# Kernel tuning notes

Measured on AMD Instinct MI355X. Metric: run time of the kernel, lower is better.

## Reference

```python
import jax, jax.numpy as jnp
import numpy as np

N_NODES = 500_000
N_EDGES = 16_000_000
D_COEF = 1  # init arg d
EPS = 1e-12  # F.normalize eps


def setup_inputs() -> dict:
    key = jax.random.key(0)
    k1, k2, k3 = jax.random.split(key, 3)
    theta = jax.random.normal(k1, (N_NODES, 1), dtype=jnp.float32)
    src = jax.random.randint(k2, (N_EDGES,), 0, N_NODES, dtype=jnp.int64)
    dst = jax.random.randint(k3, (N_EDGES,), 0, N_NODES, dtype=jnp.int64)
    v0 = jnp.ones((), dtype=jnp.float32)
    w0 = jnp.ones((), dtype=jnp.float32)
    return {"theta": theta, "src": src, "dst": dst, "v0": v0, "w0": w0}


def reference(theta, src, dst, v0, w0):
    # node velocity: v0 * [cos(theta), sin(theta)]  -> [N, 2]
    v = v0 * jnp.concatenate((jnp.cos(theta), jnp.sin(theta)), axis=-1)

    # edge message: dtheta = (theta_src - theta_dst) * d ; m = [cos, sin] -> [E, 2]
    dtheta = (theta[src, 0] - theta[dst, 0]) * D_COEF  # [E]
    m = jnp.stack((jnp.cos(dtheta), jnp.sin(dtheta)), axis=-1)  # [E, 2]

    # mailbox mean over incoming edges per destination node (segment mean)
    msum = jax.ops.segment_sum(m, dst, num_segments=N_NODES)  # [N, 2]
    cnt = jax.ops.segment_sum(jnp.ones((dst.shape[0],), m.dtype), dst,
                              num_segments=N_NODES)  # [N]
    mean_cs = msum / jnp.maximum(cnt, 1.0)[:, None]  # [N, 2]

    # torque: w0 * normalize(mean_cs, dim=-1)[..., 1:2]
    norm = jnp.linalg.norm(mean_cs, axis=-1, keepdims=True)
    unit = mean_cs / jnp.maximum(norm, EPS)
    torque = w0 * unit[:, 1:2]  # [N, 1]
    return v, torque
```

## Files before the change

kernel.cpp:

```cpp
#include <hip/hip_runtime.h>
#include <hip/hip_bf16.h>
#include <math.h>


#define NBITS_Q   21
#define Q_MASK    ((1u << NBITS_Q) - 1)
#define Q_SCALE   131072.0f
#define Q_INV     (1.0f / 131072.0f)
#define BIN_SHIFT 11
#define BIN_W     2048
#define NB        245
#define CAP       67584
#define K_BATCH   8192
#define EPT       8
#define SCALE_F   524288.0f
#define INV_SCALE (1.0f / 524288.0f)

__global__ void init_cursors(unsigned* __restrict__ cur) {
    int b = blockIdx.x * blockDim.x + threadIdx.x;
    if (b < 256) cur[b] = (b < NB) ? (unsigned)b * CAP : 0u;
}

__global__ __launch_bounds__(1024, 8) void bin_edges_sort(
        const float* __restrict__ theta,
        const int4* __restrict__ src4, const int4* __restrict__ dst4,
        unsigned* __restrict__ bins, unsigned* __restrict__ cursor, int E)
{
    __shared__ unsigned      sorted[K_BATCH];
    __shared__ unsigned char sbin[K_BATCH];
    __shared__ unsigned      hist[256];
    __shared__ unsigned      base[256];
    __shared__ unsigned      gbase[256];
    __shared__ unsigned      lcnt[256];

    const int tid   = threadIdx.x;
    const int bb    = blockIdx.x;
    const int e0    = bb * K_BATCH;
    const int nval  = min(K_BATCH, E - e0);
    const int E4    = E >> 2;
    const int base4 = e0 >> 2;

    if (tid < 256) { hist[tid] = 0u; lcnt[tid] = 0u; }
    __syncthreads();

    int4 sQ[EPT / 4], dQ[EPT / 4];
#pragma unroll
    for (int j = 0; j < EPT / 4; ++j) {
        const int idx4 = base4 + j * 1024 + tid;
        if (idx4 < E4) {
            sQ[j] = src4[idx4];
            dQ[j] = dst4[idx4];
        } else {
            sQ[j] = make_int4(0, 0, 0, 0);
            dQ[j] = make_int4(0, 0, 0, 0);
        }
    }
    float tq[EPT];
#pragma unroll
    for (int j = 0; j < EPT / 4; ++j) {
        tq[j * 4 + 0] = theta[sQ[j].x];
        tq[j * 4 + 1] = theta[sQ[j].y];
        tq[j * 4 + 2] = theta[sQ[j].z];
        tq[j * 4 + 3] = theta[sQ[j].w];
    }

    unsigned ent[EPT];
    unsigned bn[EPT];
#pragma unroll
    for (int j = 0; j < EPT / 4; ++j) {
        const int idx4 = base4 + j * 1024 + tid;
        const int q0   = j * 4;
        if (idx4 < E4) {
            const int dd[4] = {dQ[j].x, dQ[j].y, dQ[j].z, dQ[j].w};
#pragma unroll
            for (int k = 0; k < 4; ++k) {
                const unsigned b = (unsigned)dd[k] >> BIN_SHIFT;
                float qf = (tq[q0 + k] + 8.0f) * Q_SCALE + 0.5f;
                qf = fminf(fmaxf(qf, 0.0f), 2097151.0f);
                ent[q0 + k] = ((unsigned)(dd[k] & (BIN_W - 1)) << NBITS_Q)
                              | (unsigned)qf;
                bn[q0 + k]  = b;
                atomicAdd(&hist[b], 1u);
            }
        } else {
#pragma unroll
            for (int k = 0; k < 4; ++k) bn[q0 + k] = 0xFFu;
        }
    }
    __syncthreads();

    if (tid < 64) {
        unsigned h[4];
#pragma unroll
        for (int k = 0; k < 4; ++k) h[k] = hist[tid * 4 + k];
        const unsigned tot = h[0] + h[1] + h[2] + h[3];
        unsigned s = tot;
#pragma unroll
        for (int off = 1; off < 64; off <<= 1) {
            const unsigned y = __shfl_up(s, off);
            if (tid >= off) s += y;
        }
        unsigned run = s - tot;
#pragma unroll
        for (int k = 0; k < 4; ++k) {
            base[tid * 4 + k] = run;
            run += h[k];
        }
#pragma unroll
        for (int k = 0; k < 4; ++k)
            if (h[k]) gbase[tid * 4 + k] = atomicAdd(&cursor[tid * 4 + k], h[k]);
    }
    __syncthreads();

#pragma unroll
    for (int q = 0; q < EPT; ++q) {
        if (bn[q] != 0xFFu) {
            const unsigned b   = bn[q];
            const unsigned pos = base[b] + atomicAdd(&lcnt[b], 1u);
            sorted[pos] = ent[q];
            sbin[pos]   = (unsigned char)b;
        }
    }
    __syncthreads();

    for (int l = tid; l < nval; l += 1024) {
        const unsigned b    = sbin[l];
        const unsigned gpos = gbase[b] + ((unsigned)l - base[b]);
        if (gpos < (b + 1u) * CAP)
            bins[gpos] = sorted[l];
    }
}

__global__ __launch_bounds__(1024) void reduce_bins(
        const float* __restrict__ theta, const unsigned* __restrict__ bins,
        const unsigned* __restrict__ cursor, const float* __restrict__ v0p,
        const float* __restrict__ w0p, float* __restrict__ out, int N)
{
    __shared__ float th[BIN_W];
    __shared__ unsigned long long acc[BIN_W];
    const int b     = blockIdx.x;
    const int tid   = threadIdx.x;
    const int node0 = b * BIN_W;
    const int W     = min(BIN_W, N - node0);

    for (int j = tid; j < BIN_W; j += 1024) {
        th[j]  = (j < W) ? theta[node0 + j] : 0.f;
        acc[j] = 0ull;
    }
    __syncthreads();

    const unsigned  base  = (unsigned)b * CAP;
    const int       count = (int)(cursor[b] - base);
    const unsigned* bp    = bins + base;

    const int CH = 1024 * 8;
    int i0 = 0;
    for (; i0 + CH <= count; i0 += CH) {
        const uint4 ea = *(const uint4*)(bp + i0 + tid * 4);
        const uint4 eb = *(const uint4*)(bp + i0 + 4096 + tid * 4);
        const unsigned ee[8] = {ea.x, ea.y, ea.z, ea.w, eb.x, eb.y, eb.z, eb.w};
#pragma unroll
        for (int k = 0; k < 8; ++k) {
            const unsigned e = ee[k];
            const unsigned l = e >> NBITS_Q;
            const float ts = (float)(e & Q_MASK) * Q_INV - 8.0f;
            float sn, cs;
            __sincosf(ts - th[l], &sn, &cs);
            const unsigned cq = (unsigned)((cs + 1.0f) * SCALE_F + 0.5f);
            const unsigned sq = (unsigned)((sn + 1.0f) * SCALE_F + 0.5f);
            atomicAdd(&acc[l], (1ull << 56) | ((unsigned long long)cq << 28)
                               | (unsigned long long)sq);
        }
    }
    for (int i = i0 + tid; i < count; i += 1024) {
        const unsigned e = bp[i];
        const unsigned l = e >> NBITS_Q;
        const float ts = (float)(e & Q_MASK) * Q_INV - 8.0f;
        float sn, cs;
        __sincosf(ts - th[l], &sn, &cs);
        const unsigned cq = (unsigned)((cs + 1.0f) * SCALE_F + 0.5f);
        const unsigned sq = (unsigned)((sn + 1.0f) * SCALE_F + 0.5f);
        atomicAdd(&acc[l], (1ull << 56) | ((unsigned long long)cq << 28)
                           | (unsigned long long)sq);
    }
    __syncthreads();

    const float v0 = *v0p, w0 = *w0p;
    for (int j = tid; j < W; j += 1024) {
        const float t = th[j];
        float sn, cs;
        __sincosf(t, &sn, &cs);
        ((float2*)out)[node0 + j] = make_float2(v0 * cs, v0 * sn);
        const unsigned long long P = acc[j];
        const float c  = (float)(unsigned)(P >> 56);
        const float xs = (float)(unsigned)((P >> 28) & 0xFFFFFFFull) * INV_SCALE - c;
        const float ys = (float)(unsigned)(P & 0xFFFFFFFull) * INV_SCALE - c;
        const float nrm = sqrtf(xs * xs + ys * ys);
        out[2 * N + node0 + j] = w0 * (ys / fmaxf(nrm, 1e-12f));
    }
}


__global__ void zero_ws_kernel(float4* __restrict__ ws, int n4) {
    int i = blockIdx.x * blockDim.x + threadIdx.x;
    if (i < n4) ws[i] = make_float4(0.f, 0.f, 0.f, 0.f);
}

__global__ void edge_kernel_fb(const float* __restrict__ theta,
                               const int4* __restrict__ src4,
                               const int4* __restrict__ dst4,
                               float2* __restrict__ acc, int E8) {
    int i = blockIdx.x * blockDim.x + threadIdx.x;
    if (i >= E8) return;
    const int4 s0 = src4[2 * i], s1 = src4[2 * i + 1];
    const int4 d0 = dst4[2 * i], d1 = dst4[2 * i + 1];
    const int ss[8] = {s0.x, s0.y, s0.z, s0.w, s1.x, s1.y, s1.z, s1.w};
    const int dd[8] = {d0.x, d0.y, d0.z, d0.w, d1.x, d1.y, d1.z, d1.w};
    float ts[8], td[8];
#pragma unroll
    for (int k = 0; k < 8; ++k) ts[k] = theta[ss[k]];
#pragma unroll
    for (int k = 0; k < 8; ++k) td[k] = theta[dd[k]];
#pragma unroll
    for (int k = 0; k < 8; ++k) {
        float sn, cs;
        __sincosf(ts[k] - td[k], &sn, &cs);
        atomicAdd(&acc[dd[k]].x, cs);
        atomicAdd(&acc[dd[k]].y, sn);
    }
}

__global__ void node_kernel_fb(const float* __restrict__ theta,
                               const float2* __restrict__ acc,
                               const float* __restrict__ v0p,
                               const float* __restrict__ w0p,
                               float* __restrict__ out, int N) {
    int i = blockIdx.x * blockDim.x + threadIdx.x;
    if (i >= N) return;
    const float v0 = *v0p, w0 = *w0p;
    float sn, cs;
    __sincosf(theta[i], &sn, &cs);
    ((float2*)out)[i] = make_float2(v0 * cs, v0 * sn);
    const float2 a = acc[i];
    const float nrm = sqrtf(a.x * a.x + a.y * a.y);
    out[2 * N + i] = w0 * (a.y / fmaxf(nrm, 1e-12f));
}

extern "C" void kernel_launch(void* const* d_in, const int* in_sizes, int n_in,
                              void* d_out, int out_size, void* d_ws, size_t ws_size,
                              hipStream_t stream) {
    const float* theta = (const float*)d_in[0];
    const int*   src   = (const int*)d_in[1];
    const int*   dst   = (const int*)d_in[2];
    const float* v0p   = (const float*)d_in[3];
    const float* w0p   = (const float*)d_in[4];
    float*       out   = (float*)d_out;

    const int N = in_sizes[0];
    const int E = in_sizes[1];

    const size_t need = 1024 + (size_t)NB * CAP * sizeof(unsigned);

    if (ws_size >= need && N <= NB * BIN_W) {
        unsigned* cursor = (unsigned*)d_ws;
        unsigned* bins   = cursor + 256;

        init_cursors<<<1, 256, 0, stream>>>(cursor);

        const int nblk = (E + K_BATCH - 1) / K_BATCH;
        bin_edges_sort<<<nblk, 1024, 0, stream>>>(theta, (const int4*)src,
                                                  (const int4*)dst,
                                                  bins, cursor, E);

        const int nbins = (N + BIN_W - 1) / BIN_W;
        reduce_bins<<<nbins, 1024, 0, stream>>>(theta, bins, cursor,
                                                v0p, w0p, out, N);
    } else {
        float2* acc = (float2*)d_ws;
        {
            const int n4 = (2 * N) / 4;
            zero_ws_kernel<<<(n4 + 255) / 256, 256, 0, stream>>>((float4*)d_ws, n4);
        }
        {
            const int E8 = E / 8;
            edge_kernel_fb<<<(E8 + 255) / 256, 256, 0, stream>>>(
                theta, (const int4*)src, (const int4*)dst, acc, E8);
        }
        node_kernel_fb<<<(N + 255) / 256, 256, 0, stream>>>(theta, acc, v0p, w0p,
                                                            out, N);
    }
}
```

Before: 304.5 us.

## Store source index in bins and gather theta in reduce stage

The binning kernel no longer gathers theta for each edge. It packs the raw 19-bit source index with the local destination index, and the reduce kernel gathers theta[src] itself, which removes the random gather and the quantisation from the sort pass and makes theta exact. The sort kernel now runs with 256 threads per block and 32 edges per thread. The bin traffic uses nontemporal loads and stores, and sincos is replaced by the hardware sin/cos builtins on pre-scaled revolutions. The cost is that the random theta gathers move into the reduce kernel, which has only 245 blocks, and a new guard requires N to fit in 19 bits.

```diff
diff --git a/kernel.cpp b/kernel.cpp
--- a/kernel.cpp
+++ b/kernel.cpp
@@ -3,26 +3,26 @@
 #include <math.h>
 
 
-#define NBITS_Q   21
-#define Q_MASK    ((1u << NBITS_Q) - 1)
-#define Q_SCALE   131072.0f
-#define Q_INV     (1.0f / 131072.0f)
+#define NBITS_S   19
+#define SRC_MASK  ((1u << NBITS_S) - 1)
 #define BIN_SHIFT 11
 #define BIN_W     2048
 #define NB        245
 #define CAP       67584
 #define K_BATCH   8192
-#define EPT       8
+#define EPT       32
 #define SCALE_F   524288.0f
 #define INV_SCALE (1.0f / 524288.0f)
+#define INV_2PI   0.15915494309189535f
+
+typedef unsigned uint4_v __attribute__((ext_vector_type(4)));
 
 __global__ void init_cursors(unsigned* __restrict__ cur) {
     int b = blockIdx.x * blockDim.x + threadIdx.x;
     if (b < 256) cur[b] = (b < NB) ? (unsigned)b * CAP : 0u;
 }
 
-__global__ __launch_bounds__(1024, 8) void bin_edges_sort(
-        const float* __restrict__ theta,
+__global__ __launch_bounds__(256) void bin_edges_sort(
         const int4* __restrict__ src4, const int4* __restrict__ dst4,
         unsigned* __restrict__ bins, unsigned* __restrict__ cursor, int E)
 {
@@ -40,13 +40,14 @@
     const int E4    = E >> 2;
     const int base4 = e0 >> 2;
 
-    if (tid < 256) { hist[tid] = 0u; lcnt[tid] = 0u; }
+    hist[tid] = 0u;
+    lcnt[tid] = 0u;
     __syncthreads();
 
     int4 sQ[EPT / 4], dQ[EPT / 4];
 #pragma unroll
     for (int j = 0; j < EPT / 4; ++j) {
-        const int idx4 = base4 + j * 1024 + tid;
+        const int idx4 = base4 + j * 256 + tid;
         if (idx4 < E4) {
             sQ[j] = src4[idx4];
             dQ[j] = dst4[idx4];
@@ -55,30 +56,21 @@
             dQ[j] = make_int4(0, 0, 0, 0);
         }
     }
-    float tq[EPT];
-#pragma unroll
-    for (int j = 0; j < EPT / 4; ++j) {
-        tq[j * 4 + 0] = theta[sQ[j].x];
-        tq[j * 4 + 1] = theta[sQ[j].y];
-        tq[j * 4 + 2] = theta[sQ[j].z];
-        tq[j * 4 + 3] = theta[sQ[j].w];
-    }
 
     unsigned ent[EPT];
     unsigned bn[EPT];
 #pragma unroll
     for (int j = 0; j < EPT / 4; ++j) {
-        const int idx4 = base4 + j * 1024 + tid;
+        const int idx4 = base4 + j * 256 + tid;
         const int q0   = j * 4;
         if (idx4 < E4) {
             const int dd[4] = {dQ[j].x, dQ[j].y, dQ[j].z, dQ[j].w};
+            const int ss[4] = {sQ[j].x, sQ[j].y, sQ[j].z, sQ[j].w};
 #pragma unroll
             for (int k = 0; k < 4; ++k) {
                 const unsigned b = (unsigned)dd[k] >> BIN_SHIFT;
-                float qf = (tq[q0 + k] + 8.0f) * Q_SCALE + 0.5f;
-                qf = fminf(fmaxf(qf, 0.0f), 2097151.0f);
-                ent[q0 + k] = ((unsigned)(dd[k] & (BIN_W - 1)) << NBITS_Q)
-                              | (unsigned)qf;
+                ent[q0 + k] = ((unsigned)(dd[k] & (BIN_W - 1)) << NBITS_S)
+                              | (unsigned)ss[k];
                 bn[q0 + k]  = b;
                 atomicAdd(&hist[b], 1u);
             }
@@ -123,11 +115,11 @@
     }
     __syncthreads();
 
-    for (int l = tid; l < nval; l += 1024) {
+    for (int l = tid; l < nval; l += 256) {
         const unsigned b    = sbin[l];
         const unsigned gpos = gbase[b] + ((unsigned)l - base[b]);
         if (gpos < (b + 1u) * CAP)
-            bins[gpos] = sorted[l];
+            __builtin_nontemporal_store(sorted[l], &bins[gpos]);
     }
 }
 
@@ -156,16 +148,20 @@
     const int CH = 1024 * 8;
     int i0 = 0;
     for (; i0 + CH <= count; i0 += CH) {
-        const uint4 ea = *(const uint4*)(bp + i0 + tid * 4);
-        const uint4 eb = *(const uint4*)(bp + i0 + 4096 + tid * 4);
+        const uint4_v ea = __builtin_nontemporal_load(
+            (const uint4_v*)(bp + i0 + tid * 4));
+        const uint4_v eb = __builtin_nontemporal_load(
+            (const uint4_v*)(bp + i0 + 4096 + tid * 4));
         const unsigned ee[8] = {ea.x, ea.y, ea.z, ea.w, eb.x, eb.y, eb.z, eb.w};
+        float ts[8];
+#pragma unroll
+        for (int k = 0; k < 8; ++k) ts[k] = theta[ee[k] & SRC_MASK];
 #pragma unroll
         for (int k = 0; k < 8; ++k) {
-            const unsigned e = ee[k];
-            const unsigned l = e >> NBITS_Q;
-            const float ts = (float)(e & Q_MASK) * Q_INV - 8.0f;
-            float sn, cs;
-            __sincosf(ts - th[l], &sn, &cs);
+            const unsigned l = ee[k] >> NBITS_S;
+            const float r  = (ts[k] - th[l]) * INV_2PI;
+            const float sn = __builtin_amdgcn_sinf(r);
+            const float cs = __builtin_amdgcn_cosf(r);
             const unsigned cq = (unsigned)((cs + 1.0f) * SCALE_F + 0.5f);
             const unsigned sq = (unsigned)((sn + 1.0f) * SCALE_F + 0.5f);
             atomicAdd(&acc[l], (1ull << 56) | ((unsigned long long)cq << 28)
@@ -173,11 +169,12 @@
         }
     }
     for (int i = i0 + tid; i < count; i += 1024) {
-        const unsigned e = bp[i];
-        const unsigned l = e >> NBITS_Q;
-        const float ts = (float)(e & Q_MASK) * Q_INV - 8.0f;
-        float sn, cs;
-        __sincosf(ts - th[l], &sn, &cs);
+        const unsigned e = __builtin_nontemporal_load(bp + i);
+        const unsigned l = e >> NBITS_S;
+        const float ts = theta[e & SRC_MASK];
+        const float r  = (ts - th[l]) * INV_2PI;
+        const float sn = __builtin_amdgcn_sinf(r);
+        const float cs = __builtin_amdgcn_cosf(r);
         const unsigned cq = (unsigned)((cs + 1.0f) * SCALE_F + 0.5f);
         const unsigned sq = (unsigned)((sn + 1.0f) * SCALE_F + 0.5f);
         atomicAdd(&acc[l], (1ull << 56) | ((unsigned long long)cq << 28)
@@ -188,8 +185,9 @@
     const float v0 = *v0p, w0 = *w0p;
     for (int j = tid; j < W; j += 1024) {
         const float t = th[j];
-        float sn, cs;
-        __sincosf(t, &sn, &cs);
+        const float rr = t * INV_2PI;
+        const float sn = __builtin_amdgcn_sinf(rr);
+        const float cs = __builtin_amdgcn_cosf(rr);
         ((float2*)out)[node0 + j] = make_float2(v0 * cs, v0 * sn);
         const unsigned long long P = acc[j];
         const float c  = (float)(unsigned)(P >> 56);
@@ -261,16 +259,16 @@
 
     const size_t need = 1024 + (size_t)NB * CAP * sizeof(unsigned);
 
-    if (ws_size >= need && N <= NB * BIN_W) {
+    if (ws_size >= need && N <= NB * BIN_W && N <= (1 << NBITS_S)) {
         unsigned* cursor = (unsigned*)d_ws;
         unsigned* bins   = cursor + 256;
 
         init_cursors<<<1, 256, 0, stream>>>(cursor);
 
         const int nblk = (E + K_BATCH - 1) / K_BATCH;
-        bin_edges_sort<<<nblk, 1024, 0, stream>>>(theta, (const int4*)src,
-                                                  (const int4*)dst,
-                                                  bins, cursor, E);
+        bin_edges_sort<<<nblk, 256, 0, stream>>>((const int4*)src,
+                                                 (const int4*)dst,
+                                                 bins, cursor, E);
 
         const int nbins = (N + BIN_W - 1) / BIN_W;
         reduce_bins<<<nbins, 1024, 0, stream>>>(theta, bins, cursor,
```

Result: slower. 366.5 us (+20.4%).
